# Kernel tuning notes

Hardware: AMD Instinct MI355X
Metric: run time of the kernel (lower is better)

Reference implementation:

```python
import jax, jax.numpy as jnp
import numpy as np

N_HEAD, D_MODEL, D_K, D_V = 16, 1024, 64, 64
LN_EPS = 1e-5


def setup_inputs() -> dict:
    key = jax.random.key(0)
    ks = jax.random.split(key, 10)
    B, S = 2, 2048
    s = 1.0 / np.sqrt(D_MODEL)
    return {
        "q": jax.random.normal(ks[0], (B, S, D_MODEL), jnp.float32),
        "k": jax.random.normal(ks[1], (B, S, D_MODEL), jnp.float32),
        "v": jax.random.normal(ks[2], (B, S, D_MODEL), jnp.float32),
        "w_q": jax.random.normal(ks[3], (D_MODEL, N_HEAD * D_K), jnp.float32) * s,
        "w_k": jax.random.normal(ks[4], (D_MODEL, N_HEAD * D_K), jnp.float32) * s,
        "w_v": jax.random.normal(ks[5], (D_MODEL, N_HEAD * D_V), jnp.float32) * s,
        "w_fc": jax.random.normal(ks[6], (N_HEAD * D_V, D_MODEL), jnp.float32) * s,
        "b_fc": jnp.zeros((D_MODEL,), jnp.float32),
        "ln_g": jnp.ones((D_MODEL,), jnp.float32),
        "ln_b": jnp.zeros((D_MODEL,), jnp.float32),
    }


def _mha(q, k, v, w_q, w_k, w_v, w_fc, b_fc, ln_g, ln_b):
    B, S, _ = q.shape
    residual = q
    # projections -> [B, H, S, Dh]
    qh = (q @ w_q).reshape(B, S, N_HEAD, D_K).transpose(0, 2, 1, 3)
    kh = (k @ w_k).reshape(B, S, N_HEAD, D_K).transpose(0, 2, 1, 3)
    vh = (v @ w_v).reshape(B, S, N_HEAD, D_V).transpose(0, 2, 1, 3)
    # NOTE: original scales by sqrt(d_model), not sqrt(d_k)
    temper = jnp.sqrt(jnp.asarray(D_MODEL, qh.dtype))
    attn = jnp.einsum("bhqd,bhkd->bhqk", qh, kh) / temper
    attn = jax.nn.softmax(attn, axis=-1)  # dropout = identity (eval mode)
    out = jnp.einsum("bhqk,bhkd->bhqd", attn, vh)
    out = out.transpose(0, 2, 1, 3).reshape(B, S, N_HEAD * D_V)
    out = out @ w_fc + b_fc  # dropout = identity (eval mode)
    x = out + residual
    mu = jnp.mean(x, axis=-1, keepdims=True)
    var = jnp.var(x, axis=-1, keepdims=True)
    x = (x - mu) * jax.lax.rsqrt(var + LN_EPS) * ln_g + ln_b
    return x, attn


def reference(q, k, v, w_q, w_k, w_v, w_fc, b_fc, ln_g, ln_b):
    return _mha(q, k, v, w_q, w_k, w_v, w_fc, b_fc, ln_g, ln_b)
```

## Files before the change

kernel.cpp:

```cpp
#include <hip/hip_runtime.h>
#include <hip/hip_bf16.h>
#include <stdint.h>

typedef __attribute__((ext_vector_type(8))) short bf16x8;
typedef __attribute__((ext_vector_type(4))) float f32x4;

#define GLOAD16(gptr, lptr)                                              \
  __builtin_amdgcn_global_load_lds(                                      \
      (const __attribute__((address_space(1))) void*)(gptr),             \
      (__attribute__((address_space(3))) void*)(lptr), 16, 0, 0)

__device__ __forceinline__ uint32_t pack_bf16_2(float a, float b) {
  union { __hip_bfloat16 h; unsigned short u; } ca, cb;
  ca.h = __float2bfloat16(a); cb.h = __float2bfloat16(b);
  return (uint32_t)ca.u | ((uint32_t)cb.u << 16);
}

__global__ __launch_bounds__(256)
void cvt_kernel(const float* __restrict__ in0, const float* __restrict__ in1,
                const float* __restrict__ in2, __hip_bfloat16* __restrict__ out0,
                __hip_bfloat16* __restrict__ out1, __hip_bfloat16* __restrict__ out2,
                int n)
{
  const int z = blockIdx.y;
  const float* in = z == 0 ? in0 : z == 1 ? in1 : in2;
  __hip_bfloat16* out = z == 0 ? out0 : z == 1 ? out1 : out2;
  long i = ((long)blockIdx.x * 256 + threadIdx.x) * 8;
  if (i + 8 > n) return;
  float4 a = *(const float4*)(in + i);
  float4 b = *(const float4*)(in + i + 4);
  uint4 r;
  r.x = pack_bf16_2(a.x, a.y); r.y = pack_bf16_2(a.z, a.w);
  r.z = pack_bf16_2(b.x, b.y); r.w = pack_bf16_2(b.z, b.w);
  *(uint4*)(out + i) = r;
}

__global__ __launch_bounds__(256)
void wtrans_kernel(const float* __restrict__ w0, const float* __restrict__ w1,
                   const float* __restrict__ w2, const float* __restrict__ w3,
                   __hip_bfloat16* __restrict__ o0, __hip_bfloat16* __restrict__ o1,
                   __hip_bfloat16* __restrict__ o2, __hip_bfloat16* __restrict__ o3)
{
  const int z = blockIdx.z;
  const float* in = z == 0 ? w0 : z == 1 ? w1 : z == 2 ? w2 : w3;
  __hip_bfloat16* out = z == 0 ? o0 : z == 1 ? o1 : z == 2 ? o2 : o3;
  __shared__ float t[64][65];
  const int tx = threadIdx.x & 15, ty = threadIdx.x >> 4;
  const int bx = blockIdx.x, by = blockIdx.y;
  for (int i = 0; i < 4; ++i)
    for (int j = 0; j < 4; ++j)
      t[ty*4+i][tx*4+j] = in[(long)(by*64 + ty*4+i)*1024 + bx*64 + tx*4 + j];
  __syncthreads();
  for (int i = 0; i < 4; ++i)
    for (int j = 0; j < 4; ++j)
      out[(long)(bx*64 + ty*4+i)*1024 + by*64 + tx*4 + j] =
          __float2bfloat16(t[tx*4+j][ty*4+i]);
}

__global__ __launch_bounds__(256)
void vtrans_kernel(const __hip_bfloat16* __restrict__ in, __hip_bfloat16* __restrict__ out)
{
  __shared__ __hip_bfloat16 t[64][72];
  const int tx = threadIdx.x & 15, ty = threadIdx.x >> 4;
  const int sb = blockIdx.x, bh = blockIdx.y;
  const __hip_bfloat16* inp = in + (long)bh * 2048 * 64;
  __hip_bfloat16* outp = out + (long)bh * 64 * 2048;
  for (int i = 0; i < 4; ++i)
    for (int j = 0; j < 4; ++j)
      t[ty*4+i][tx*4+j] = inp[(long)(sb*64 + ty*4+i)*64 + tx*4 + j];
  __syncthreads();
  for (int i = 0; i < 4; ++i)
    for (int j = 0; j < 4; ++j)
      outp[(long)(ty*4+i)*2048 + sb*64 + tx*4 + j] = t[tx*4+j][ty*4+i];
}

template<int EPI>
__global__ __launch_bounds__(256)
void gemm_bt(const __hip_bfloat16* __restrict__ A0,
             const __hip_bfloat16* __restrict__ A1,
             const __hip_bfloat16* __restrict__ A2,
             const __hip_bfloat16* __restrict__ B0,
             const __hip_bfloat16* __restrict__ B1,
             const __hip_bfloat16* __restrict__ B2,
             void* __restrict__ out,
             const float* __restrict__ bias,
             const float* __restrict__ resid,
             int M, int N, int K)
{
  const int z = (EPI == 0) ? blockIdx.z : 0;
  const __hip_bfloat16* A  = z == 0 ? A0 : z == 1 ? A1 : A2;
  const __hip_bfloat16* Bt = z == 0 ? B0 : z == 1 ? B1 : B2;
  const float scale = (EPI == 0 && z == 0) ? 0.045084219f : 1.0f;

  __shared__ __hip_bfloat16 As[128*32];
  __shared__ __hip_bfloat16 Bs[128*32];
  const int tid = threadIdx.x;
  const int wid = tid >> 6;
  const int lane = tid & 63;
  const int lr = lane & 15, lg = lane >> 4;
  const int bm = blockIdx.y, bn = blockIdx.x;
  const int wm = wid >> 1, wn = wid & 1;

  f32x4 acc[4][4] = {};

  const int srow = tid >> 2;
  const int scol = (tid & 3) * 8;
  const __hip_bfloat16* Ag = A  + (long)(bm*128 + srow)*K + scol;
  const __hip_bfloat16* Bg = Bt + (long)(bn*128 + srow)*K + scol;
  __hip_bfloat16* AsW = &As[wid*512];
  __hip_bfloat16* BsW = &Bs[wid*512];

  for (int k0 = 0; k0 < K; k0 += 32) {
    GLOAD16(Ag + k0,          AsW);
    GLOAD16(Ag + 64*K + k0,   AsW + 2048);
    GLOAD16(Bg + k0,          BsW);
    GLOAD16(Bg + 64*K + k0,   BsW + 2048);
    __syncthreads();
    bf16x8 a[4], b[4];
    for (int m = 0; m < 4; ++m)
      a[m] = *(const bf16x8*)&As[(wm*64 + m*16 + lr)*32 + lg*8];
    for (int n = 0; n < 4; ++n)
      b[n] = *(const bf16x8*)&Bs[(wn*64 + n*16 + lr)*32 + lg*8];
    for (int m = 0; m < 4; ++m)
      for (int n = 0; n < 4; ++n)
        acc[m][n] = __builtin_amdgcn_mfma_f32_16x16x32_bf16(b[n], a[m], acc[m][n], 0, 0, 0);
    __syncthreads();
  }

  for (int m = 0; m < 4; ++m) {
    const int grow = bm*128 + wm*64 + m*16 + lr;
    for (int n = 0; n < 4; ++n) {
      const int c0 = bn*128 + wn*64 + n*16 + lg*4;
      if (EPI == 0) {
        const int b_ = grow >> 11, s = grow & 2047;
        const int h = c0 >> 6, d = c0 & 63;
        uint2 pk;
        pk.x = pack_bf16_2(acc[m][n][0]*scale, acc[m][n][1]*scale);
        pk.y = pack_bf16_2(acc[m][n][2]*scale, acc[m][n][3]*scale);
        *(uint2*)((__hip_bfloat16*)out + (long)z*4194304 +
                  ((long)(b_*16 + h)*2048 + s)*64 + d) = pk;
      } else {
        float4 b4 = *(const float4*)(bias + c0);
        float4 r4 = *(const float4*)(resid + (long)grow*N + c0);
        float4 o4;
        o4.x = acc[m][n][0] + b4.x + r4.x;
        o4.y = acc[m][n][1] + b4.y + r4.y;
        o4.z = acc[m][n][2] + b4.z + r4.z;
        o4.w = acc[m][n][3] + b4.w + r4.w;
        *(float4*)((float*)out + (long)grow*N + c0) = o4;
      }
    }
  }
}

__global__ __launch_bounds__(256)
void attn_kernel(const __hip_bfloat16* __restrict__ Qh,
                 const __hip_bfloat16* __restrict__ Kh,
                 const __hip_bfloat16* __restrict__ Vt,
                 float* __restrict__ attn_out,
                 __hip_bfloat16* __restrict__ O)
{
  __shared__ __hip_bfloat16 Ps[2][64*128];
  __shared__ float red[4][64];
  __shared__ float invl[64];

  const int tid = threadIdx.x, wid = tid >> 6, lane = tid & 63;
  const int lr = lane & 15, lg = lane >> 4;
  const int orig = (blockIdx.x & 7) * 128 + (blockIdx.x >> 3);
  const int bh = orig >> 5, qb = orig & 31;

  const __hip_bfloat16* Qlane = Qh + ((long)bh*2048 + qb*64 + lr)*64 + lg*8;
  const __hip_bfloat16* Klane = Kh + (long)bh*2048*64 + (long)(wid*32 + lr)*64 + lg*8;
  const __hip_bfloat16* Vlane = Vt + (long)bh*64*2048 + (long)(wid*16 + lr)*2048 + lg*8;

  bf16x8 aq[4][2];
  for (int mq = 0; mq < 4; ++mq)
    for (int kk = 0; kk < 2; ++kk)
      aq[mq][kk] = *(const bf16x8*)(Qlane + mq*1024 + kk*32);

  float rs[4] = {0.f, 0.f, 0.f, 0.f};
  for (int kt = 0; kt < 16; ++kt) {
    bf16x8 bk[2][2];
    for (int nk = 0; nk < 2; ++nk)
      for (int kk = 0; kk < 2; ++kk)
        bk[nk][kk] = *(const bf16x8*)(Klane + kt*8192 + nk*1024 + kk*32);
    f32x4 s2[4][2] = {};
    for (int mq = 0; mq < 4; ++mq)
      for (int nk = 0; nk < 2; ++nk)
        for (int kk = 0; kk < 2; ++kk)
          s2[mq][nk] = __builtin_amdgcn_mfma_f32_16x16x32_bf16(bk[nk][kk], aq[mq][kk], s2[mq][nk], 0, 0, 0);
    for (int mq = 0; mq < 4; ++mq)
      for (int nk = 0; nk < 2; ++nk)
        for (int jj = 0; jj < 4; ++jj)
          rs[mq] += exp2f(s2[mq][nk][jj]);
  }

  for (int mq = 0; mq < 4; ++mq) {
    float e = rs[mq];
    e += __shfl_xor(e, 16);
    e += __shfl_xor(e, 32);
    rs[mq] = e;
  }
  if (lg == 0)
    for (int mq = 0; mq < 4; ++mq)
      red[wid][mq*16 + lr] = rs[mq];
  __syncthreads();
  if (tid < 64)
    invl[tid] = 1.0f / (red[0][tid] + red[1][tid] + red[2][tid] + red[3][tid]);
  __syncthreads();

  float iv[4];
  for (int mq = 0; mq < 4; ++mq) iv[mq] = invl[mq*16 + lr];

  f32x4 acc_o[4] = {};
  float* attn_row = attn_out + ((long)bh*2048 + qb*64)*2048;

  bf16x8 bk[2][2], vb[4];
#pragma unroll
  for (int nk = 0; nk < 2; ++nk)
    for (int kk = 0; kk < 2; ++kk)
      bk[nk][kk] = *(const bf16x8*)(Klane + nk*1024 + kk*32);
#pragma unroll
  for (int k2 = 0; k2 < 4; ++k2)
    vb[k2] = *(const bf16x8*)(Vlane + k2*32);

#pragma unroll 1
  for (int kt = 0; kt < 16; ++kt) {
    __hip_bfloat16* Pbuf = Ps[kt & 1];
    f32x4 s2[4][2] = {};
    __builtin_amdgcn_s_setprio(1);
#pragma unroll
    for (int mq = 0; mq < 4; ++mq)
      for (int nk = 0; nk < 2; ++nk)
        for (int kk = 0; kk < 2; ++kk)
          s2[mq][nk] = __builtin_amdgcn_mfma_f32_16x16x32_bf16(bk[nk][kk], aq[mq][kk], s2[mq][nk], 0, 0, 0);
    __builtin_amdgcn_s_setprio(0);

    bf16x8 nbk[2][2], nvb[4];
    if (kt < 15) {
#pragma unroll
      for (int nk = 0; nk < 2; ++nk)
        for (int kk = 0; kk < 2; ++kk)
          nbk[nk][kk] = *(const bf16x8*)(Klane + (kt+1)*8192 + nk*1024 + kk*32);
#pragma unroll
      for (int k2 = 0; k2 < 4; ++k2)
        nvb[k2] = *(const bf16x8*)(Vlane + (kt+1)*128 + k2*32);
    }

#pragma unroll
    for (int mq = 0; mq < 4; ++mq) {
      const int row = mq*16 + lr;
      for (int nk = 0; nk < 2; ++nk) {
        const int kc = wid*32 + nk*16 + lg*4;
        f32x4 p;
        p[0] = exp2f(s2[mq][nk][0]) * iv[mq];
        p[1] = exp2f(s2[mq][nk][1]) * iv[mq];
        p[2] = exp2f(s2[mq][nk][2]) * iv[mq];
        p[3] = exp2f(s2[mq][nk][3]) * iv[mq];
        __builtin_nontemporal_store(p, (f32x4*)(attn_row + (long)row*2048 + kt*128 + kc));
        uint2 pb;
        pb.x = pack_bf16_2(p[0], p[1]);
        pb.y = pack_bf16_2(p[2], p[3]);
        const int boff = (row*256 + kc*2) ^ ((row & 15) << 4);
        *(uint2*)((char*)Pbuf + boff) = pb;
      }
    }

    asm volatile("s_waitcnt lgkmcnt(0)" ::: "memory");
    __builtin_amdgcn_sched_barrier(0);
    __builtin_amdgcn_s_barrier();
    __builtin_amdgcn_sched_barrier(0);

    __builtin_amdgcn_s_setprio(1);
#pragma unroll
    for (int mq = 0; mq < 4; ++mq) {
      const int row = mq*16 + lr;
      for (int k2 = 0; k2 < 4; ++k2) {
        const int boff = (row*256 + (k2*32 + lg*8)*2) ^ ((row & 15) << 4);
        bf16x8 pa = *(const bf16x8*)((char*)Pbuf + boff);
        acc_o[mq] = __builtin_amdgcn_mfma_f32_16x16x32_bf16(vb[k2], pa, acc_o[mq], 0, 0, 0);
      }
    }
    __builtin_amdgcn_s_setprio(0);

#pragma unroll
    for (int nk = 0; nk < 2; ++nk)
      for (int kk = 0; kk < 2; ++kk)
        bk[nk][kk] = nbk[nk][kk];
#pragma unroll
    for (int k2 = 0; k2 < 4; ++k2)
      vb[k2] = nvb[k2];
  }

  const int b_ = bh >> 4, h = bh & 15;
  for (int mq = 0; mq < 4; ++mq) {
    const long grow = (long)b_*2048 + qb*64 + mq*16 + lr;
    const int col = h*64 + wid*16 + lg*4;
    uint2 pk;
    pk.x = pack_bf16_2(acc_o[mq][0], acc_o[mq][1]);
    pk.y = pack_bf16_2(acc_o[mq][2], acc_o[mq][3]);
    *(uint2*)(O + grow*1024 + col) = pk;
  }
}

__global__ __launch_bounds__(256)
void ln_kernel(const float* __restrict__ xin, const float* __restrict__ gam,
               const float* __restrict__ bet, float* __restrict__ xout)
{
  const int row = blockIdx.x;
  const int tid = threadIdx.x;
  const float* xr = xin + (long)row*1024;
  float4 v = *(const float4*)(xr + tid*4);
  float s  = v.x + v.y + v.z + v.w;
  float ss = v.x*v.x + v.y*v.y + v.z*v.z + v.w*v.w;
  for (int o = 1; o < 64; o <<= 1) {
    s  += __shfl_xor(s, o, 64);
    ss += __shfl_xor(ss, o, 64);
  }
  __shared__ float rsh[4], rssh[4];
  const int wid = tid >> 6, lane = tid & 63;
  if (lane == 0) { rsh[wid] = s; rssh[wid] = ss; }
  __syncthreads();
  s  = rsh[0] + rsh[1] + rsh[2] + rsh[3];
  ss = rssh[0] + rssh[1] + rssh[2] + rssh[3];
  const float mean = s * (1.0f/1024.0f);
  const float var  = ss * (1.0f/1024.0f) - mean*mean;
  const float rstd = rsqrtf(var + 1e-5f);
  float4 g4 = *(const float4*)(gam + tid*4);
  float4 b4 = *(const float4*)(bet + tid*4);
  float4 o4;
  o4.x = (v.x - mean)*rstd*g4.x + b4.x;
  o4.y = (v.y - mean)*rstd*g4.y + b4.y;
  o4.z = (v.z - mean)*rstd*g4.z + b4.z;
  o4.w = (v.w - mean)*rstd*g4.w + b4.w;
  *(float4*)(xout + (long)row*1024 + tid*4) = o4;
}

extern "C" void kernel_launch(void* const* d_in, const int* in_sizes, int n_in,
                              void* d_out, int out_size, void* d_ws, size_t ws_size,
                              hipStream_t stream)
{
  (void)in_sizes; (void)n_in; (void)out_size; (void)ws_size;
  const float* q    = (const float*)d_in[0];
  const float* k    = (const float*)d_in[1];
  const float* v    = (const float*)d_in[2];
  const float* w_q  = (const float*)d_in[3];
  const float* w_k  = (const float*)d_in[4];
  const float* w_v  = (const float*)d_in[5];
  const float* w_fc = (const float*)d_in[6];
  const float* b_fc = (const float*)d_in[7];
  const float* ln_g = (const float*)d_in[8];
  const float* ln_b = (const float*)d_in[9];

  const long MB = 1024*1024;
  char* ws = (char*)d_ws;
  __hip_bfloat16* q_bf  = (__hip_bfloat16*)(ws);
  __hip_bfloat16* k_bf  = (__hip_bfloat16*)(ws +  8*MB);
  __hip_bfloat16* v_bf  = (__hip_bfloat16*)(ws + 16*MB);
  __hip_bfloat16* wq_t  = (__hip_bfloat16*)(ws + 24*MB);
  __hip_bfloat16* wk_t  = (__hip_bfloat16*)(ws + 26*MB);
  __hip_bfloat16* wv_t  = (__hip_bfloat16*)(ws + 28*MB);
  __hip_bfloat16* wfc_t = (__hip_bfloat16*)(ws + 30*MB);
  __hip_bfloat16* QKVh  = (__hip_bfloat16*)(ws + 32*MB);
  __hip_bfloat16* Qh    = QKVh;
  __hip_bfloat16* Kh    = QKVh + 4194304L;
  __hip_bfloat16* Vh    = QKVh + 8388608L;
  __hip_bfloat16* Vht   = (__hip_bfloat16*)(ws + 56*MB);
  __hip_bfloat16* Obuf  = (__hip_bfloat16*)(ws + 64*MB);
  float*          xbuf  = (float*)(ws + 72*MB);

  float* x_out    = (float*)d_out;
  float* attn_out = x_out + 4194304L;

  const int NQ = 4096*1024;
  cvt_kernel<<<dim3(NQ/2048, 3), 256, 0, stream>>>(q, k, v, q_bf, k_bf, v_bf, NQ);

  wtrans_kernel<<<dim3(16, 16, 4), 256, 0, stream>>>(w_q, w_k, w_v, w_fc,
                                                     wq_t, wk_t, wv_t, wfc_t);

  gemm_bt<0><<<dim3(8, 32, 3), 256, 0, stream>>>(q_bf, k_bf, v_bf,
                                                 wq_t, wk_t, wv_t,
                                                 QKVh, nullptr, nullptr, 4096, 1024, 1024);

  vtrans_kernel<<<dim3(32, 32), 256, 0, stream>>>(Vh, Vht);

  attn_kernel<<<1024, 256, 0, stream>>>(Qh, Kh, Vht, attn_out, Obuf);

  gemm_bt<2><<<dim3(8, 32), 256, 0, stream>>>(Obuf, nullptr, nullptr,
                                              wfc_t, nullptr, nullptr,
                                              xbuf, b_fc, q, 4096, 1024, 1024);

  ln_kernel<<<4096, 256, 0, stream>>>(xbuf, ln_g, ln_b, x_out);
}
```

Baseline: 279.6 us.

## Split attention block into two 32-row halves, overlapping second half's row-sum pass

Each 64-query block is now processed as two 32-row halves. The row-sum (first) pass for the second half is folded into the output pass of the first half, so that half's QK MFMAs share K loads with the first half's work. LDS use is halved, and the explicit register prefetch of the next K/V tile is removed in favour of in-loop loads. The aim is to hide one full score-recompute pass and to lower LDS and register pressure, but the loop body loses its software prefetch and gains extra barriers.

```diff
diff --git a/kernel.cpp b/kernel.cpp
--- a/kernel.cpp
+++ b/kernel.cpp
@@ -160,104 +160,190 @@
                  float* __restrict__ attn_out,
                  __hip_bfloat16* __restrict__ O)
 {
-  __shared__ __hip_bfloat16 Ps[2][64*128];
-  __shared__ float red[4][64];
-  __shared__ float invl[64];
+  __shared__ __hip_bfloat16 Ps[2][32*128];
+  __shared__ float red[4][32];
+  __shared__ float invl[2][32];
 
   const int tid = threadIdx.x, wid = tid >> 6, lane = tid & 63;
   const int lr = lane & 15, lg = lane >> 4;
   const int orig = (blockIdx.x & 7) * 128 + (blockIdx.x >> 3);
-  const int bh = orig >> 5, qb = orig & 31;
-
-  const __hip_bfloat16* Qlane = Qh + ((long)bh*2048 + qb*64 + lr)*64 + lg*8;
+  const int bh = orig >> 5, qp = orig & 31;
+
+  const __hip_bfloat16* Qlane = Qh + ((long)bh*2048 + qp*64 + lr)*64 + lg*8;
   const __hip_bfloat16* Klane = Kh + (long)bh*2048*64 + (long)(wid*32 + lr)*64 + lg*8;
   const __hip_bfloat16* Vlane = Vt + (long)bh*64*2048 + (long)(wid*16 + lr)*2048 + lg*8;
 
-  bf16x8 aq[4][2];
-  for (int mq = 0; mq < 4; ++mq)
-    for (int kk = 0; kk < 2; ++kk)
-      aq[mq][kk] = *(const bf16x8*)(Qlane + mq*1024 + kk*32);
-
-  float rs[4] = {0.f, 0.f, 0.f, 0.f};
+  bf16x8 aqa[2][2], aqb[2][2];
+  for (int mq = 0; mq < 2; ++mq)
+    for (int kk = 0; kk < 2; ++kk) {
+      aqa[mq][kk] = *(const bf16x8*)(Qlane + mq*1024 + kk*32);
+      aqb[mq][kk] = *(const bf16x8*)(Qlane + 2048 + mq*1024 + kk*32);
+    }
+
+  float rsa[2] = {0.f, 0.f};
   for (int kt = 0; kt < 16; ++kt) {
     bf16x8 bk[2][2];
     for (int nk = 0; nk < 2; ++nk)
       for (int kk = 0; kk < 2; ++kk)
         bk[nk][kk] = *(const bf16x8*)(Klane + kt*8192 + nk*1024 + kk*32);
-    f32x4 s2[4][2] = {};
-    for (int mq = 0; mq < 4; ++mq)
+    f32x4 s2[2][2] = {};
+    for (int mq = 0; mq < 2; ++mq)
       for (int nk = 0; nk < 2; ++nk)
         for (int kk = 0; kk < 2; ++kk)
-          s2[mq][nk] = __builtin_amdgcn_mfma_f32_16x16x32_bf16(bk[nk][kk], aq[mq][kk], s2[mq][nk], 0, 0, 0);
-    for (int mq = 0; mq < 4; ++mq)
+          s2[mq][nk] = __builtin_amdgcn_mfma_f32_16x16x32_bf16(bk[nk][kk], aqa[mq][kk], s2[mq][nk], 0, 0, 0);
+    for (int mq = 0; mq < 2; ++mq)
       for (int nk = 0; nk < 2; ++nk)
         for (int jj = 0; jj < 4; ++jj)
-          rs[mq] += exp2f(s2[mq][nk][jj]);
-  }
-
-  for (int mq = 0; mq < 4; ++mq) {
-    float e = rs[mq];
+          rsa[mq] += exp2f(s2[mq][nk][jj]);
+  }
+  for (int mq = 0; mq < 2; ++mq) {
+    float e = rsa[mq];
     e += __shfl_xor(e, 16);
     e += __shfl_xor(e, 32);
-    rs[mq] = e;
+    rsa[mq] = e;
   }
   if (lg == 0)
-    for (int mq = 0; mq < 4; ++mq)
-      red[wid][mq*16 + lr] = rs[mq];
-  __syncthreads();
-  if (tid < 64)
-    invl[tid] = 1.0f / (red[0][tid] + red[1][tid] + red[2][tid] + red[3][tid]);
-  __syncthreads();
-
-  float iv[4];
-  for (int mq = 0; mq < 4; ++mq) iv[mq] = invl[mq*16 + lr];
-
-  f32x4 acc_o[4] = {};
-  float* attn_row = attn_out + ((long)bh*2048 + qb*64)*2048;
-
-  bf16x8 bk[2][2], vb[4];
-#pragma unroll
-  for (int nk = 0; nk < 2; ++nk)
-    for (int kk = 0; kk < 2; ++kk)
-      bk[nk][kk] = *(const bf16x8*)(Klane + nk*1024 + kk*32);
-#pragma unroll
-  for (int k2 = 0; k2 < 4; ++k2)
-    vb[k2] = *(const bf16x8*)(Vlane + k2*32);
+    for (int mq = 0; mq < 2; ++mq)
+      red[wid][mq*16 + lr] = rsa[mq];
+  __syncthreads();
+  if (tid < 32)
+    invl[0][tid] = 1.0f / (red[0][tid] + red[1][tid] + red[2][tid] + red[3][tid]);
+  __syncthreads();
+
+  float iva[2];
+  for (int mq = 0; mq < 2; ++mq) iva[mq] = invl[0][mq*16 + lr];
+
+  f32x4 acc_oa[2] = {};
+  float rsb[2] = {0.f, 0.f};
+  float* rowA = attn_out + ((long)bh*2048 + qp*64)*2048;
 
 #pragma unroll 1
   for (int kt = 0; kt < 16; ++kt) {
     __hip_bfloat16* Pbuf = Ps[kt & 1];
-    f32x4 s2[4][2] = {};
+    bf16x8 bk[2][2], vb[4];
+#pragma unroll
+    for (int nk = 0; nk < 2; ++nk)
+      for (int kk = 0; kk < 2; ++kk)
+        bk[nk][kk] = *(const bf16x8*)(Klane + kt*8192 + nk*1024 + kk*32);
+#pragma unroll
+    for (int k2 = 0; k2 < 4; ++k2)
+      vb[k2] = *(const bf16x8*)(Vlane + kt*128 + k2*32);
+
+    f32x4 s2a[2][2] = {}, s2b[2][2] = {};
     __builtin_amdgcn_s_setprio(1);
 #pragma unroll
-    for (int mq = 0; mq < 4; ++mq)
+    for (int mq = 0; mq < 2; ++mq)
       for (int nk = 0; nk < 2; ++nk)
-        for (int kk = 0; kk < 2; ++kk)
-          s2[mq][nk] = __builtin_amdgcn_mfma_f32_16x16x32_bf16(bk[nk][kk], aq[mq][kk], s2[mq][nk], 0, 0, 0);
+        for (int kk = 0; kk < 2; ++kk) {
+          s2a[mq][nk] = __builtin_amdgcn_mfma_f32_16x16x32_bf16(bk[nk][kk], aqa[mq][kk], s2a[mq][nk], 0, 0, 0);
+          s2b[mq][nk] = __builtin_amdgcn_mfma_f32_16x16x32_bf16(bk[nk][kk], aqb[mq][kk], s2b[mq][nk], 0, 0, 0);
+        }
     __builtin_amdgcn_s_setprio(0);
 
-    bf16x8 nbk[2][2], nvb[4];
-    if (kt < 15) {
-#pragma unroll
-      for (int nk = 0; nk < 2; ++nk)
-        for (int kk = 0; kk < 2; ++kk)
-          nbk[nk][kk] = *(const bf16x8*)(Klane + (kt+1)*8192 + nk*1024 + kk*32);
-#pragma unroll
-      for (int k2 = 0; k2 < 4; ++k2)
-        nvb[k2] = *(const bf16x8*)(Vlane + (kt+1)*128 + k2*32);
-    }
-
-#pragma unroll
-    for (int mq = 0; mq < 4; ++mq) {
+#pragma unroll
+    for (int mq = 0; mq < 2; ++mq) {
       const int row = mq*16 + lr;
       for (int nk = 0; nk < 2; ++nk) {
         const int kc = wid*32 + nk*16 + lg*4;
         f32x4 p;
-        p[0] = exp2f(s2[mq][nk][0]) * iv[mq];
-        p[1] = exp2f(s2[mq][nk][1]) * iv[mq];
-        p[2] = exp2f(s2[mq][nk][2]) * iv[mq];
-        p[3] = exp2f(s2[mq][nk][3]) * iv[mq];
-        __builtin_nontemporal_store(p, (f32x4*)(attn_row + (long)row*2048 + kt*128 + kc));
+        p[0] = exp2f(s2a[mq][nk][0]) * iva[mq];
+        p[1] = exp2f(s2a[mq][nk][1]) * iva[mq];
+        p[2] = exp2f(s2a[mq][nk][2]) * iva[mq];
+        p[3] = exp2f(s2a[mq][nk][3]) * iva[mq];
+        __builtin_nontemporal_store(p, (f32x4*)(rowA + (long)row*2048 + kt*128 + kc));
+        uint2 pb;
+        pb.x = pack_bf16_2(p[0], p[1]);
+        pb.y = pack_bf16_2(p[2], p[3]);
+        const int boff = (row*256 + kc*2) ^ ((row & 15) << 4);
+        *(uint2*)((char*)Pbuf + boff) = pb;
+        rsb[mq] += exp2f(s2b[mq][nk][0]) + exp2f(s2b[mq][nk][1])
+                 + exp2f(s2b[mq][nk][2]) + exp2f(s2b[mq][nk][3]);
+      }
+    }
+
+    asm volatile("s_waitcnt lgkmcnt(0)" ::: "memory");
+    __builtin_amdgcn_sched_barrier(0);
+    __builtin_amdgcn_s_barrier();
+    __builtin_amdgcn_sched_barrier(0);
+
+    __builtin_amdgcn_s_setprio(1);
+#pragma unroll
+    for (int mq = 0; mq < 2; ++mq) {
+      const int row = mq*16 + lr;
+      for (int k2 = 0; k2 < 4; ++k2) {
+        const int boff = (row*256 + (k2*32 + lg*8)*2) ^ ((row & 15) << 4);
+        bf16x8 pa = *(const bf16x8*)((char*)Pbuf + boff);
+        acc_oa[mq] = __builtin_amdgcn_mfma_f32_16x16x32_bf16(vb[k2], pa, acc_oa[mq], 0, 0, 0);
+      }
+    }
+    __builtin_amdgcn_s_setprio(0);
+  }
+
+  {
+    const int b_ = bh >> 4, h = bh & 15;
+    for (int mq = 0; mq < 2; ++mq) {
+      const long grow = (long)b_*2048 + qp*64 + mq*16 + lr;
+      const int col = h*64 + wid*16 + lg*4;
+      uint2 pk;
+      pk.x = pack_bf16_2(acc_oa[mq][0], acc_oa[mq][1]);
+      pk.y = pack_bf16_2(acc_oa[mq][2], acc_oa[mq][3]);
+      *(uint2*)(O + grow*1024 + col) = pk;
+    }
+  }
+
+  for (int mq = 0; mq < 2; ++mq) {
+    float e = rsb[mq];
+    e += __shfl_xor(e, 16);
+    e += __shfl_xor(e, 32);
+    rsb[mq] = e;
+  }
+  __syncthreads();
+  if (lg == 0)
+    for (int mq = 0; mq < 2; ++mq)
+      red[wid][mq*16 + lr] = rsb[mq];
+  __syncthreads();
+  if (tid < 32)
+    invl[1][tid] = 1.0f / (red[0][tid] + red[1][tid] + red[2][tid] + red[3][tid]);
+  __syncthreads();
+
+  float ivb[2];
+  for (int mq = 0; mq < 2; ++mq) ivb[mq] = invl[1][mq*16 + lr];
+
+  f32x4 acc_ob[2] = {};
+  float* rowB = attn_out + ((long)bh*2048 + qp*64 + 32)*2048;
+
+#pragma unroll 1
+  for (int kt = 0; kt < 16; ++kt) {
+    __hip_bfloat16* Pbuf = Ps[kt & 1];
+    bf16x8 bk[2][2], vb[4];
+#pragma unroll
+    for (int nk = 0; nk < 2; ++nk)
+      for (int kk = 0; kk < 2; ++kk)
+        bk[nk][kk] = *(const bf16x8*)(Klane + kt*8192 + nk*1024 + kk*32);
+#pragma unroll
+    for (int k2 = 0; k2 < 4; ++k2)
+      vb[k2] = *(const bf16x8*)(Vlane + kt*128 + k2*32);
+
+    f32x4 s2[2][2] = {};
+    __builtin_amdgcn_s_setprio(1);
+#pragma unroll
+    for (int mq = 0; mq < 2; ++mq)
+      for (int nk = 0; nk < 2; ++nk)
+        for (int kk = 0; kk < 2; ++kk)
+          s2[mq][nk] = __builtin_amdgcn_mfma_f32_16x16x32_bf16(bk[nk][kk], aqb[mq][kk], s2[mq][nk], 0, 0, 0);
+    __builtin_amdgcn_s_setprio(0);
+
+#pragma unroll
+    for (int mq = 0; mq < 2; ++mq) {
+      const int row = mq*16 + lr;
+      for (int nk = 0; nk < 2; ++nk) {
+        const int kc = wid*32 + nk*16 + lg*4;
+        f32x4 p;
+        p[0] = exp2f(s2[mq][nk][0]) * ivb[mq];
+        p[1] = exp2f(s2[mq][nk][1]) * ivb[mq];
+        p[2] = exp2f(s2[mq][nk][2]) * ivb[mq];
+        p[3] = exp2f(s2[mq][nk][3]) * ivb[mq];
+        __builtin_nontemporal_store(p, (f32x4*)(rowB + (long)row*2048 + kt*128 + kc));
         uint2 pb;
         pb.x = pack_bf16_2(p[0], p[1]);
         pb.y = pack_bf16_2(p[2], p[3]);
@@ -273,33 +359,27 @@
 
     __builtin_amdgcn_s_setprio(1);
 #pragma unroll
-    for (int mq = 0; mq < 4; ++mq) {
+    for (int mq = 0; mq < 2; ++mq) {
       const int row = mq*16 + lr;
       for (int k2 = 0; k2 < 4; ++k2) {
         const int boff = (row*256 + (k2*32 + lg*8)*2) ^ ((row & 15) << 4);
         bf16x8 pa = *(const bf16x8*)((char*)Pbuf + boff);
-        acc_o[mq] = __builtin_amdgcn_mfma_f32_16x16x32_bf16(vb[k2], pa, acc_o[mq], 0, 0, 0);
+        acc_ob[mq] = __builtin_amdgcn_mfma_f32_16x16x32_bf16(vb[k2], pa, acc_ob[mq], 0, 0, 0);
       }
     }
     __builtin_amdgcn_s_setprio(0);
-
-#pragma unroll
-    for (int nk = 0; nk < 2; ++nk)
-      for (int kk = 0; kk < 2; ++kk)
-        bk[nk][kk] = nbk[nk][kk];
-#pragma unroll
-    for (int k2 = 0; k2 < 4; ++k2)
-      vb[k2] = nvb[k2];
-  }
-
-  const int b_ = bh >> 4, h = bh & 15;
-  for (int mq = 0; mq < 4; ++mq) {
-    const long grow = (long)b_*2048 + qb*64 + mq*16 + lr;
-    const int col = h*64 + wid*16 + lg*4;
-    uint2 pk;
-    pk.x = pack_bf16_2(acc_o[mq][0], acc_o[mq][1]);
-    pk.y = pack_bf16_2(acc_o[mq][2], acc_o[mq][3]);
-    *(uint2*)(O + grow*1024 + col) = pk;
+  }
+
+  {
+    const int b_ = bh >> 4, h = bh & 15;
+    for (int mq = 0; mq < 2; ++mq) {
+      const long grow = (long)b_*2048 + qp*64 + 32 + mq*16 + lr;
+      const int col = h*64 + wid*16 + lg*4;
+      uint2 pk;
+      pk.x = pack_bf16_2(acc_ob[mq][0], acc_ob[mq][1]);
+      pk.y = pack_bf16_2(acc_ob[mq][2], acc_ob[mq][3]);
+      *(uint2*)(O + grow*1024 + col) = pk;
+    }
   }
 }
 
```

After: 338.1 us. 21.0% more time.
